# Performance work log

Measured on AMD Instinct MI355X. Metric: run time of the kernel, lower is better.

## Reference

```python
import jax, jax.numpy as jnp
import numpy as np

B, S, D, H, DH = 4, 2048, 512, 8, 64  # batch, seq, input_dim, heads, per-head output_dim


def setup_inputs() -> dict:
    key = jax.random.key(0)
    ks = jax.random.split(key, 10)
    scale = 0.02
    inp = {
        "x": jax.random.normal(ks[0], (B, S, D), dtype=jnp.float32),
        "biological_mask": jnp.ones((B, S), dtype=bool),
        "Wq": jax.random.normal(ks[1], (D, H * DH), dtype=jnp.float32) * scale,
        "bq": jnp.zeros((H * DH,), dtype=jnp.float32),
        "Wk": jax.random.normal(ks[2], (D, H * DH), dtype=jnp.float32) * scale,
        "bk": jnp.zeros((H * DH,), dtype=jnp.float32),
        "Wv": jax.random.normal(ks[3], (D, H * DH), dtype=jnp.float32) * scale,
        "bv": jnp.zeros((H * DH,), dtype=jnp.float32),
        "Wo": jax.random.normal(ks[4], (H * DH, DH), dtype=jnp.float32) * scale,
        "bo": jnp.zeros((DH,), dtype=jnp.float32),
        "prior_weight": jnp.full((1,), 0.1, dtype=jnp.float32),
    }
    return inp


def reference(x, biological_mask, Wq, bq, Wk, bk, Wv, bv, Wo, bo, prior_weight):
    b, s, _ = x.shape
    inv_sqrt_dh = jnp.float32(1.0 / np.sqrt(DH))
    # projections -> [B,H,S,DH]
    q = (x @ Wq + bq).reshape(b, s, H, DH).transpose(0, 2, 1, 3)
    k = (x @ Wk + bk).reshape(b, s, H, DH).transpose(0, 2, 1, 3)
    v = (x @ Wv + bv).reshape(b, s, H, DH).transpose(0, 2, 1, 3)
    # scores [B,H,S,S]
    scores = jnp.einsum("bhqd,bhkd->bhqk", q, k) * inv_sqrt_dh
    # biological prior: identity matrix, broadcast over batch and heads
    prior = jnp.eye(s, dtype=scores.dtype)[None, None, :, :]
    scores = scores + prior_weight[0] * prior
    attn = jax.nn.softmax(scores, axis=-1)  # dropout is identity in eval mode
    attended = jnp.einsum("bhqk,bhkd->bhqd", attn, v)
    attended = attended.transpose(0, 2, 1, 3).reshape(b, s, H * DH)
    return attended @ Wo + bo
```

## Files before the change

kernel.cpp:

```cpp
#include <hip/hip_runtime.h>
#include <hip/hip_bf16.h>

#define B_ 4
#define S_ 2048
#define D_ 512
#define H_ 8
#define DH_ 64
#define HD_ 512
#define M_ 8192
#define QKVN 1536
#define QKN 1024
#define LOG2E 1.4426950408889634f

typedef __attribute__((ext_vector_type(8))) short bf16x8;
typedef __attribute__((ext_vector_type(4))) float f32x4;
typedef unsigned short u16;

__device__ inline u16 f2bf(float f) {
    __hip_bfloat16 h = __float2bfloat16(f);
    return *reinterpret_cast<u16*>(&h);
}

__device__ inline void async_cp16(const void* g, void* l) {
    __builtin_amdgcn_global_load_lds(
        (const __attribute__((address_space(1))) unsigned int*)g,
        (__attribute__((address_space(3))) unsigned int*)l, 16, 0, 0);
}

__global__ __launch_bounds__(256) void prep_all(
    const float* __restrict__ x, const float* __restrict__ Wq,
    const float* __restrict__ Wk, const float* __restrict__ Wv,
    const float* __restrict__ Wo, u16* __restrict__ xb,
    u16* __restrict__ WqkvT, u16* __restrict__ WoT)
{
    const int z = blockIdx.z;
    const int tid = threadIdx.x;

    if (z == 4) {
        const int id = blockIdx.y * 64 + blockIdx.x;
#pragma unroll
        for (int it = 0; it < 4; ++it) {
            int i = it * 131072 + id * 256 + tid;
            float4 a = *reinterpret_cast<const float4*>(&x[(size_t)i * 8]);
            float4 b = *reinterpret_cast<const float4*>(&x[(size_t)i * 8 + 4]);
            bf16x8 o;
            o[0] = f2bf(a.x); o[1] = f2bf(a.y); o[2] = f2bf(a.z); o[3] = f2bf(a.w);
            o[4] = f2bf(b.x); o[5] = f2bf(b.y); o[6] = f2bf(b.z); o[7] = f2bf(b.w);
            *reinterpret_cast<bf16x8*>(&xb[(size_t)i * 8]) = o;
        }
        return;
    }

    const float* src; u16* dst; int R, C;
    if (z < 3) { if (blockIdx.x >= 8) return;
                 src = (z == 0) ? Wq : (z == 1) ? Wk : Wv;
                 dst = WqkvT + (size_t)z * 512 * 512; R = 512; C = 512; }
    else       { if (blockIdx.x) return; src = Wo; dst = WoT; R = 512; C = 64; }

    __shared__ u16 T[64][65];
    const int c0 = blockIdx.x * 64, r0 = blockIdx.y * 64;
#pragma unroll
    for (int i = 0; i < 4; ++i) {
        int idx = i * 256 + tid;
        int r = idx >> 4, q4 = (idx & 15) << 2;
        float4 vv = *reinterpret_cast<const float4*>(&src[(size_t)(r0 + r) * C + c0 + q4]);
        T[r][q4 + 0] = f2bf(vv.x); T[r][q4 + 1] = f2bf(vv.y);
        T[r][q4 + 2] = f2bf(vv.z); T[r][q4 + 3] = f2bf(vv.w);
    }
    __syncthreads();
#pragma unroll
    for (int i = 0; i < 2; ++i) {
        int idx = i * 256 + tid;
        int cc = idx >> 3, jj = idx & 7;
        bf16x8 o;
#pragma unroll
        for (int e = 0; e < 8; ++e) o[e] = (short)T[jj * 8 + e][cc];
        *reinterpret_cast<bf16x8*>(&dst[(size_t)(c0 + cc) * R + r0 + jj * 8]) = o;
    }
}

__global__ __launch_bounds__(256) void gemm_qkv(
    const u16* __restrict__ A, const u16* __restrict__ BT,
    const float* __restrict__ bq, const float* __restrict__ bk,
    const float* __restrict__ bv, u16* __restrict__ qk,
    u16* __restrict__ v3, float qscale)
{
    __shared__ __align__(16) u16 As[128 * 64];
    __shared__ __align__(16) u16 Bs[128 * 64];
    const int tid = threadIdx.x, lane = tid & 63, w = tid >> 6;
    const int l15 = lane & 15, l4 = lane >> 4;

    const int bidf = blockIdx.x;
    const int xcd = bidf & 7, pos = bidf >> 3;
    const int swz = xcd * 96 + pos;
    const int by = swz / 12, bx = swz - by * 12;
    const int tm = by * 128, tn = bx * 128;
    const int wm = (w >> 1) * 64, wn = (w & 1) * 64;

    f32x4 acc[4][4] = {};

    for (int k0 = 0; k0 < 512; k0 += 64) {
#pragma unroll
        for (int i = 0; i < 4; ++i) {
            int call = w * 4 + i;
            int c = call * 64 + lane;
            int r = c >> 3, j = c & 7;
            async_cp16(A + (size_t)(tm + r) * 512 + k0 + ((j ^ (r & 7)) << 3),
                       &As[call * 512]);
            async_cp16(BT + (size_t)(tn + r) * 512 + k0 + ((j ^ (r & 7)) << 3),
                       &Bs[call * 512]);
        }
        __syncthreads();
#pragma unroll
        for (int ks = 0; ks < 2; ++ks) {
            bf16x8 af[4], bf[4];
#pragma unroll
            for (int mf = 0; mf < 4; ++mf) {
                int r = wm + mf * 16 + l15;
                int j = ks * 4 + l4;
                af[mf] = *reinterpret_cast<const bf16x8*>(&As[(r * 8 + (j ^ (r & 7))) * 8]);
            }
#pragma unroll
            for (int nf = 0; nf < 4; ++nf) {
                int r = wn + nf * 16 + l15;
                int j = ks * 4 + l4;
                bf[nf] = *reinterpret_cast<const bf16x8*>(&Bs[(r * 8 + (j ^ (r & 7))) * 8]);
            }
#pragma unroll
            for (int mf = 0; mf < 4; ++mf)
#pragma unroll
                for (int nf = 0; nf < 4; ++nf)
                    acc[mf][nf] = __builtin_amdgcn_mfma_f32_16x16x32_bf16(
                        af[mf], bf[nf], acc[mf][nf], 0, 0, 0);
        }
        __syncthreads();
    }
#pragma unroll
    for (int nf = 0; nf < 4; ++nf) {
        const int col = tn + wn + nf * 16 + l15;
        if (col < QKN) {
            const float bias_v = (col < 512) ? bq[col] : bk[col - 512];
            const float scl = (col < 512) ? qscale : 1.0f;
#pragma unroll
            for (int mf = 0; mf < 4; ++mf)
#pragma unroll
                for (int r = 0; r < 4; ++r) {
                    int row = tm + wm + mf * 16 + l4 * 4 + r;
                    qk[(size_t)row * QKN + col] = f2bf((acc[mf][nf][r] + bias_v) * scl);
                }
        } else {
            const int dcol = col - QKN;
            const float bias_v = bv[dcol];
            const int hh = dcol >> 6, d64 = dcol & 63;
            const int n = d64 >> 4, dd = d64 & 15;
#pragma unroll
            for (int mf = 0; mf < 4; ++mf) {
                int row0 = tm + wm + mf * 16 + l4 * 4;
                int b = row0 >> 11, s = row0 & 2047;
                int t = s >> 6, s6 = s & 63;
                int ks = s6 >> 5, l4i = (s6 >> 3) & 3, kvi = s6 & 7;
                ushort4 pk;
                pk.x = f2bf(acc[mf][nf][0] + bias_v);
                pk.y = f2bf(acc[mf][nf][1] + bias_v);
                pk.z = f2bf(acc[mf][nf][2] + bias_v);
                pk.w = f2bf(acc[mf][nf][3] + bias_v);
                size_t idx = (((((size_t)(b * 8 + hh) * 32 + t) * 4 + n) * 2 + ks) * 4
                              + l4i) * 128 + dd * 8 + kvi;
                *reinterpret_cast<ushort4*>(&v3[idx]) = pk;
            }
        }
    }
}

__global__ __launch_bounds__(256, 4) void flash_mfma(
    const u16* __restrict__ qk, const u16* __restrict__ v3,
    const float* __restrict__ pw_ptr, u16* __restrict__ att)
{
    __shared__ __align__(16) u16 Kb[2][8192];

    const int tid = threadIdx.x, lane = tid & 63, w = tid >> 6;
    const int l15 = lane & 15, l4 = lane >> 4;
    const int bid = blockIdx.x;
    const int x = bid & 7, g = bid >> 3;
    const int bh = x * 4 + (g >> 5), qt = g & 31;
    const int h = bh & 7, b = bh >> 3;
    const float pwl = pw_ptr[0] * LOG2E;

    const u16* qbase = qk + (size_t)b * S_ * QKN + h * 64;
    const u16* kbase = qbase + 512;
    const u16* vbase = v3 + (size_t)bh * 32 * 4 * 2 * 512 + l4 * 128 + l15 * 8;

    const int qrow0 = qt * 64 + w * 16;
    bf16x8 qb[2];
#pragma unroll
    for (int ks2 = 0; ks2 < 2; ++ks2)
        qb[ks2] = *reinterpret_cast<const bf16x8*>(
            &qbase[(size_t)(qrow0 + l15) * QKN + ks2 * 32 + l4 * 8]);

    const bf16x8 ones = {(short)0x3F80, (short)0x3F80, (short)0x3F80, (short)0x3F80,
                         (short)0x3F80, (short)0x3F80, (short)0x3F80, (short)0x3F80};

    f32x4 accv[4] = {};
    f32x4 accl = {};

#define STAGE2(buf, jj) do {                                                       \
    _Pragma("unroll")                                                              \
    for (int i_ = 0; i_ < 4; ++i_) {                                               \
        int call_ = w * 4 + i_;                                                    \
        int c_ = call_ * 64 + lane;                                                \
        int rho_ = c_ >> 3, j_ = c_ & 7;                                           \
        int r6_ = rho_ & 63;                                                       \
        int pi_ = (rho_ & 64) | (r6_ & 32) | ((r6_ & 12) << 1)                     \
                | ((r6_ & 16) >> 2) | (r6_ & 3);                                   \
        async_cp16(kbase + (size_t)((jj) + pi_) * QKN + ((j_ ^ (r6_ & 7)) << 3),   \
                   &Kb[buf][call_ * 512]);                                         \
    } } while (0)

    STAGE2(0, 0);
    __syncthreads();
    int cur = 0;

    for (int t = 0; t < 16; ++t) {
        if (t < 15) STAGE2(cur ^ 1, (t + 1) << 7);

#pragma unroll
        for (int half = 0; half < 2; ++half) {
            const int t2 = t * 2 + half;
            const int j0h = t2 << 6;
            const u16* vt = vbase + (size_t)t2 * 4096;
            const u16* kb = &Kb[cur][half * 4096];

            bf16x8 vb01[2][2];
#pragma unroll
            for (int n = 0; n < 2; ++n)
#pragma unroll
                for (int ks = 0; ks < 2; ++ks)
                    vb01[n][ks] = *reinterpret_cast<const bf16x8*>(
                        vt + (n * 2 + ks) * 512);

            f32x4 s[4] = {};
            __builtin_amdgcn_s_setprio(1);
#pragma unroll
            for (int c = 0; c < 4; ++c)
#pragma unroll
                for (int ks2 = 0; ks2 < 2; ++ks2) {
                    const int rr = c * 16 + l15;
                    const int sl = ks2 * 4 + l4;
                    bf16x8 ka = *reinterpret_cast<const bf16x8*>(
                        &kb[(rr * 8 + (sl ^ (rr & 7))) * 8]);
                    s[c] = __builtin_amdgcn_mfma_f32_16x16x32_bf16(ka, qb[ks2], s[c], 0, 0, 0);
                }
            __builtin_amdgcn_s_setprio(0);

            bf16x8 vb23[2][2];
#pragma unroll
            for (int n = 0; n < 2; ++n)
#pragma unroll
                for (int ks = 0; ks < 2; ++ks)
                    vb23[n][ks] = *reinterpret_cast<const bf16x8*>(
                        vt + ((n + 2) * 2 + ks) * 512);

            if (t2 == qt) {
#pragma unroll
                for (int c = 0; c < 4; ++c)
#pragma unroll
                    for (int r = 0; r < 4; ++r) {
                        int kv = (c >> 1) * 32 + l4 * 8 + (c & 1) * 4 + r;
                        if (j0h + kv == qrow0 + l15) s[c][r] += pwl;
                    }
            }

            bf16x8 pa[2];
#pragma unroll
            for (int ks = 0; ks < 2; ++ks)
#pragma unroll
                for (int d2 = 0; d2 < 2; ++d2)
#pragma unroll
                    for (int r = 0; r < 4; ++r)
                        pa[ks][d2 * 4 + r] = (short)f2bf(exp2f(s[ks * 2 + d2][r]));

            __builtin_amdgcn_s_setprio(1);
            accl = __builtin_amdgcn_mfma_f32_16x16x32_bf16(pa[0], ones, accl, 0, 0, 0);
            accl = __builtin_amdgcn_mfma_f32_16x16x32_bf16(pa[1], ones, accl, 0, 0, 0);
#pragma unroll
            for (int n = 0; n < 2; ++n)
#pragma unroll
                for (int ks = 0; ks < 2; ++ks)
                    accv[n] = __builtin_amdgcn_mfma_f32_16x16x32_bf16(
                        pa[ks], vb01[n][ks], accv[n], 0, 0, 0);
#pragma unroll
            for (int n = 0; n < 2; ++n)
#pragma unroll
                for (int ks = 0; ks < 2; ++ks)
                    accv[n + 2] = __builtin_amdgcn_mfma_f32_16x16x32_bf16(
                        pa[ks], vb23[n][ks], accv[n + 2], 0, 0, 0);
            __builtin_amdgcn_s_setprio(0);
        }

        __syncthreads();
        cur ^= 1;
    }
#undef STAGE2

#pragma unroll
    for (int r = 0; r < 4; ++r) {
        float inv = 1.0f / accl[r];
        int row = qrow0 + l4 * 4 + r;
#pragma unroll
        for (int nf = 0; nf < 4; ++nf)
            att[(size_t)(b * S_ + row) * HD_ + h * 64 + nf * 16 + l15] =
                f2bf(accv[nf][r] * inv);
    }
}

__global__ __launch_bounds__(256) void out_proj(
    const u16* __restrict__ att, const u16* __restrict__ WoT,
    const float* __restrict__ bo, float* __restrict__ out)
{
    __shared__ float red[32][65];
    const int tid = threadIdx.x, lane = tid & 63, w = tid >> 6;
    const int l15 = lane & 15, l4 = lane >> 4;
    const int row0 = blockIdx.x * 32;
    const int rsub = (w & 1) * 16, kh = w >> 1;

    f32x4 acc[4] = {};
#pragma unroll
    for (int ks = 0; ks < 8; ++ks) {
        bf16x8 a = *reinterpret_cast<const bf16x8*>(
            &att[(size_t)(row0 + rsub + l15) * 512 + (kh * 8 + ks) * 32 + l4 * 8]);
#pragma unroll
        for (int nf = 0; nf < 4; ++nf) {
            bf16x8 bb = *reinterpret_cast<const bf16x8*>(
                &WoT[(size_t)(nf * 16 + l15) * 512 + (kh * 8 + ks) * 32 + l4 * 8]);
            acc[nf] = __builtin_amdgcn_mfma_f32_16x16x32_bf16(a, bb, acc[nf], 0, 0, 0);
        }
    }
    if (kh == 1) {
#pragma unroll
        for (int nf = 0; nf < 4; ++nf)
#pragma unroll
            for (int r = 0; r < 4; ++r)
                red[rsub + l4 * 4 + r][nf * 16 + l15] = acc[nf][r];
    }
    __syncthreads();
    if (kh == 0) {
#pragma unroll
        for (int nf = 0; nf < 4; ++nf) {
            int n = nf * 16 + l15;
            float bias_v = bo[n];
#pragma unroll
            for (int r = 0; r < 4; ++r)
                out[(size_t)(row0 + rsub + l4 * 4 + r) * 64 + n] =
                    acc[nf][r] + red[rsub + l4 * 4 + r][n] + bias_v;
        }
    }
}

extern "C" void kernel_launch(void* const* d_in, const int* in_sizes, int n_in,
                              void* d_out, int out_size, void* d_ws, size_t ws_size,
                              hipStream_t stream)
{
    const float* x  = (const float*)d_in[0];
    const float* Wq = (const float*)d_in[2];
    const float* bq = (const float*)d_in[3];
    const float* Wk = (const float*)d_in[4];
    const float* bk = (const float*)d_in[5];
    const float* Wv = (const float*)d_in[6];
    const float* bv = (const float*)d_in[7];
    const float* Wo = (const float*)d_in[8];
    const float* bo = (const float*)d_in[9];
    const float* pw = (const float*)d_in[10];

    u16* ws = (u16*)d_ws;
    size_t o = 0;
    u16* xb    = ws + o; o += (size_t)M_ * D_;
    u16* WqkvT = ws + o; o += (size_t)QKVN * D_;
    u16* WoT   = ws + o; o += (size_t)DH_ * HD_;
    u16* qkb   = ws + o; o += (size_t)M_ * QKN;
    u16* v3b   = ws + o; o += (size_t)M_ * HD_;
    u16* att   = ws + o; o += (size_t)M_ * HD_;

    dim3 blk(256);
    prep_all<<<dim3(64, 8, 5), blk, 0, stream>>>(x, Wq, Wk, Wv, Wo, xb, WqkvT, WoT);

    gemm_qkv<<<dim3(768), blk, 0, stream>>>(
        xb, WqkvT, bq, bk, bv, qkb, v3b, 0.125f * LOG2E);

    flash_mfma<<<dim3(1024), blk, 0, stream>>>(qkb, v3b, pw, att);

    out_proj<<<dim3(256), blk, 0, stream>>>(att, WoT, bo, (float*)d_out);
}
```

Before: 98.87 us.

## Split attention KV range into two halves with separate combine kernel

Each query tile's KV loop is split across two blocks (split-K / flash-decoding style), doubling the grid to 2048 blocks with half the LDS per block and a higher occupancy hint. Each block writes an unnormalized bf16 partial output plus row sums, and a new combine kernel adds the two partials and normalizes. Because the softmax uses no running max (the scores are small), partials can simply be added. The aim is more parallelism and occupancy, at the cost of an extra launch, extra global traffic for the partials, and an extra bf16 rounding step.

```diff
diff --git a/kernel.cpp b/kernel.cpp
--- a/kernel.cpp
+++ b/kernel.cpp
@@ -15,10 +15,14 @@
 typedef __attribute__((ext_vector_type(8))) short bf16x8;
 typedef __attribute__((ext_vector_type(4))) float f32x4;
 typedef unsigned short u16;
+typedef unsigned int u32;
 
 __device__ inline u16 f2bf(float f) {
     __hip_bfloat16 h = __float2bfloat16(f);
     return *reinterpret_cast<u16*>(&h);
+}
+__device__ inline float bf2f(u16 u) {
+    union { u32 i; float f; } v; v.i = (u32)u << 16; return v.f;
 }
 
 __device__ inline void async_cp16(const void* g, void* l) {
@@ -172,17 +176,19 @@
     }
 }
 
-__global__ __launch_bounds__(256, 4) void flash_mfma(
+__global__ __launch_bounds__(256, 8) void flash_mfma(
     const u16* __restrict__ qk, const u16* __restrict__ v3,
-    const float* __restrict__ pw_ptr, u16* __restrict__ att)
-{
-    __shared__ __align__(16) u16 Kb[2][8192];
+    const float* __restrict__ pw_ptr, u16* __restrict__ opart,
+    float* __restrict__ lpart)
+{
+    __shared__ __align__(16) u16 Kb[2][4096];
 
     const int tid = threadIdx.x, lane = tid & 63, w = tid >> 6;
     const int l15 = lane & 15, l4 = lane >> 4;
     const int bid = blockIdx.x;
     const int x = bid & 7, g = bid >> 3;
-    const int bh = x * 4 + (g >> 5), qt = g & 31;
+    const int bh = x * 4 + (g >> 6);
+    const int rem = g & 63, qt = rem >> 1, half = rem & 1;
     const int h = bh & 7, b = bh >> 3;
     const float pwl = pw_ptr[0] * LOG2E;
 
@@ -202,114 +208,139 @@
 
     f32x4 accv[4] = {};
     f32x4 accl = {};
-
-#define STAGE2(buf, jj) do {                                                       \
+    const int t0 = half * 16;
+
+#define STAGE(buf, jj) do {                                                        \
     _Pragma("unroll")                                                              \
-    for (int i_ = 0; i_ < 4; ++i_) {                                               \
-        int call_ = w * 4 + i_;                                                    \
+    for (int i_ = 0; i_ < 2; ++i_) {                                               \
+        int call_ = w * 2 + i_;                                                    \
         int c_ = call_ * 64 + lane;                                                \
         int rho_ = c_ >> 3, j_ = c_ & 7;                                           \
-        int r6_ = rho_ & 63;                                                       \
-        int pi_ = (rho_ & 64) | (r6_ & 32) | ((r6_ & 12) << 1)                     \
-                | ((r6_ & 16) >> 2) | (r6_ & 3);                                   \
-        async_cp16(kbase + (size_t)((jj) + pi_) * QKN + ((j_ ^ (r6_ & 7)) << 3),   \
+        int pi_ = (rho_ & 32) | ((rho_ & 12) << 1) | ((rho_ & 16) >> 2)            \
+                | (rho_ & 3);                                                      \
+        async_cp16(kbase + (size_t)((jj) + pi_) * QKN + ((j_ ^ (rho_ & 7)) << 3),  \
                    &Kb[buf][call_ * 512]);                                         \
     } } while (0)
 
-    STAGE2(0, 0);
+    STAGE(0, t0 << 6);
     __syncthreads();
     int cur = 0;
 
-    for (int t = 0; t < 16; ++t) {
-        if (t < 15) STAGE2(cur ^ 1, (t + 1) << 7);
-
-#pragma unroll
-        for (int half = 0; half < 2; ++half) {
-            const int t2 = t * 2 + half;
-            const int j0h = t2 << 6;
-            const u16* vt = vbase + (size_t)t2 * 4096;
-            const u16* kb = &Kb[cur][half * 4096];
-
-            bf16x8 vb01[2][2];
-#pragma unroll
-            for (int n = 0; n < 2; ++n)
-#pragma unroll
-                for (int ks = 0; ks < 2; ++ks)
-                    vb01[n][ks] = *reinterpret_cast<const bf16x8*>(
-                        vt + (n * 2 + ks) * 512);
-
-            f32x4 s[4] = {};
-            __builtin_amdgcn_s_setprio(1);
+    for (int ti = 0; ti < 16; ++ti) {
+        const int t = t0 + ti;
+        const int j0 = t << 6;
+        const u16* vt = vbase + (size_t)t * 4096;
+
+        bf16x8 vb01[2][2];
+#pragma unroll
+        for (int n = 0; n < 2; ++n)
+#pragma unroll
+            for (int ks = 0; ks < 2; ++ks)
+                vb01[n][ks] = *reinterpret_cast<const bf16x8*>(
+                    vt + (n * 2 + ks) * 512);
+
+        if (ti < 15) STAGE(cur ^ 1, (t + 1) << 6);
+
+        f32x4 s[4] = {};
+        __builtin_amdgcn_s_setprio(1);
+#pragma unroll
+        for (int c = 0; c < 4; ++c)
+#pragma unroll
+            for (int ks2 = 0; ks2 < 2; ++ks2) {
+                const int rr = c * 16 + l15;
+                const int sl = ks2 * 4 + l4;
+                bf16x8 ka = *reinterpret_cast<const bf16x8*>(
+                    &Kb[cur][(rr * 8 + (sl ^ (rr & 7))) * 8]);
+                s[c] = __builtin_amdgcn_mfma_f32_16x16x32_bf16(ka, qb[ks2], s[c], 0, 0, 0);
+            }
+        __builtin_amdgcn_s_setprio(0);
+
+        bf16x8 vb23[2][2];
+#pragma unroll
+        for (int n = 0; n < 2; ++n)
+#pragma unroll
+            for (int ks = 0; ks < 2; ++ks)
+                vb23[n][ks] = *reinterpret_cast<const bf16x8*>(
+                    vt + ((n + 2) * 2 + ks) * 512);
+
+        if (t == qt) {
 #pragma unroll
             for (int c = 0; c < 4; ++c)
 #pragma unroll
-                for (int ks2 = 0; ks2 < 2; ++ks2) {
-                    const int rr = c * 16 + l15;
-                    const int sl = ks2 * 4 + l4;
-                    bf16x8 ka = *reinterpret_cast<const bf16x8*>(
-                        &kb[(rr * 8 + (sl ^ (rr & 7))) * 8]);
-                    s[c] = __builtin_amdgcn_mfma_f32_16x16x32_bf16(ka, qb[ks2], s[c], 0, 0, 0);
+                for (int r = 0; r < 4; ++r) {
+                    int kv = (c >> 1) * 32 + l4 * 8 + (c & 1) * 4 + r;
+                    if (j0 + kv == qrow0 + l15) s[c][r] += pwl;
                 }
-            __builtin_amdgcn_s_setprio(0);
-
-            bf16x8 vb23[2][2];
-#pragma unroll
-            for (int n = 0; n < 2; ++n)
-#pragma unroll
-                for (int ks = 0; ks < 2; ++ks)
-                    vb23[n][ks] = *reinterpret_cast<const bf16x8*>(
-                        vt + ((n + 2) * 2 + ks) * 512);
-
-            if (t2 == qt) {
-#pragma unroll
-                for (int c = 0; c < 4; ++c)
-#pragma unroll
-                    for (int r = 0; r < 4; ++r) {
-                        int kv = (c >> 1) * 32 + l4 * 8 + (c & 1) * 4 + r;
-                        if (j0h + kv == qrow0 + l15) s[c][r] += pwl;
-                    }
-            }
-
-            bf16x8 pa[2];
+        }
+
+        bf16x8 pa[2];
+#pragma unroll
+        for (int ks = 0; ks < 2; ++ks)
+#pragma unroll
+            for (int d2 = 0; d2 < 2; ++d2)
+#pragma unroll
+                for (int r = 0; r < 4; ++r)
+                    pa[ks][d2 * 4 + r] = (short)f2bf(exp2f(s[ks * 2 + d2][r]));
+
+        __builtin_amdgcn_s_setprio(1);
+        accl = __builtin_amdgcn_mfma_f32_16x16x32_bf16(pa[0], ones, accl, 0, 0, 0);
+        accl = __builtin_amdgcn_mfma_f32_16x16x32_bf16(pa[1], ones, accl, 0, 0, 0);
+#pragma unroll
+        for (int n = 0; n < 2; ++n)
 #pragma unroll
             for (int ks = 0; ks < 2; ++ks)
-#pragma unroll
-                for (int d2 = 0; d2 < 2; ++d2)
-#pragma unroll
-                    for (int r = 0; r < 4; ++r)
-                        pa[ks][d2 * 4 + r] = (short)f2bf(exp2f(s[ks * 2 + d2][r]));
-
-            __builtin_amdgcn_s_setprio(1);
-            accl = __builtin_amdgcn_mfma_f32_16x16x32_bf16(pa[0], ones, accl, 0, 0, 0);
-            accl = __builtin_amdgcn_mfma_f32_16x16x32_bf16(pa[1], ones, accl, 0, 0, 0);
-#pragma unroll
-            for (int n = 0; n < 2; ++n)
-#pragma unroll
-                for (int ks = 0; ks < 2; ++ks)
-                    accv[n] = __builtin_amdgcn_mfma_f32_16x16x32_bf16(
-                        pa[ks], vb01[n][ks], accv[n], 0, 0, 0);
-#pragma unroll
-            for (int n = 0; n < 2; ++n)
-#pragma unroll
-                for (int ks = 0; ks < 2; ++ks)
-                    accv[n + 2] = __builtin_amdgcn_mfma_f32_16x16x32_bf16(
-                        pa[ks], vb23[n][ks], accv[n + 2], 0, 0, 0);
-            __builtin_amdgcn_s_setprio(0);
-        }
+                accv[n] = __builtin_amdgcn_mfma_f32_16x16x32_bf16(
+                    pa[ks], vb01[n][ks], accv[n], 0, 0, 0);
+#pragma unroll
+        for (int n = 0; n < 2; ++n)
+#pragma unroll
+            for (int ks = 0; ks < 2; ++ks)
+                accv[n + 2] = __builtin_amdgcn_mfma_f32_16x16x32_bf16(
+                    pa[ks], vb23[n][ks], accv[n + 2], 0, 0, 0);
+        __builtin_amdgcn_s_setprio(0);
 
         __syncthreads();
         cur ^= 1;
     }
-#undef STAGE2
-
+#undef STAGE
+
+    const size_t cell = (size_t)(bh * 32 + qt) * 2 + half;
 #pragma unroll
     for (int r = 0; r < 4; ++r) {
-        float inv = 1.0f / accl[r];
-        int row = qrow0 + l4 * 4 + r;
+        const int row6 = w * 16 + l4 * 4 + r;
 #pragma unroll
         for (int nf = 0; nf < 4; ++nf)
-            att[(size_t)(b * S_ + row) * HD_ + h * 64 + nf * 16 + l15] =
-                f2bf(accv[nf][r] * inv);
+            opart[cell * 4096 + (size_t)row6 * 64 + nf * 16 + l15] =
+                f2bf(accv[nf][r]);
+        if (l15 == 0) lpart[cell * 64 + row6] = accl[r];
+    }
+}
+
+__global__ __launch_bounds__(256) void combine(
+    const u16* __restrict__ opart, const float* __restrict__ lpart,
+    u16* __restrict__ att)
+{
+    const int cp = blockIdx.x;
+    const int bh = cp >> 5, qt = cp & 31;
+    const int h = bh & 7, b = bh >> 3;
+    const int tid = threadIdx.x;
+    const int row = tid >> 2, cg = tid & 3;
+
+    const float inv = 1.0f / (lpart[(size_t)cp * 128 + row] +
+                              lpart[(size_t)cp * 128 + 64 + row]);
+    const u16* p0 = opart + (size_t)cp * 8192 + (size_t)row * 64 + cg * 16;
+    const u16* p1 = p0 + 4096;
+
+    u16* dst = att + ((size_t)(b * S_ + qt * 64 + row)) * HD_ + h * 64 + cg * 16;
+#pragma unroll
+    for (int hchunk = 0; hchunk < 2; ++hchunk) {
+        bf16x8 a = *reinterpret_cast<const bf16x8*>(p0 + hchunk * 8);
+        bf16x8 c = *reinterpret_cast<const bf16x8*>(p1 + hchunk * 8);
+        bf16x8 o;
+#pragma unroll
+        for (int e = 0; e < 8; ++e)
+            o[e] = (short)f2bf((bf2f((u16)a[e]) + bf2f((u16)c[e])) * inv);
+        *reinterpret_cast<bf16x8*>(dst + hchunk * 8) = o;
     }
 }
 
@@ -379,6 +410,8 @@
     u16* qkb   = ws + o; o += (size_t)M_ * QKN;
     u16* v3b   = ws + o; o += (size_t)M_ * HD_;
     u16* att   = ws + o; o += (size_t)M_ * HD_;
+    u16* opart = ws + o; o += (size_t)2048 * 4096;
+    float* lprt = (float*)(ws + o); o += (size_t)2048 * 64 * 2;
 
     dim3 blk(256);
     prep_all<<<dim3(64, 8, 5), blk, 0, stream>>>(x, Wq, Wk, Wv, Wo, xb, WqkvT, WoT);
@@ -386,7 +419,9 @@
     gemm_qkv<<<dim3(768), blk, 0, stream>>>(
         xb, WqkvT, bq, bk, bv, qkb, v3b, 0.125f * LOG2E);
 
-    flash_mfma<<<dim3(1024), blk, 0, stream>>>(qkb, v3b, pw, att);
+    flash_mfma<<<dim3(2048), blk, 0, stream>>>(qkb, v3b, pw, opart, lprt);
+
+    combine<<<dim3(1024), blk, 0, stream>>>(opart, lprt, att);
 
     out_proj<<<dim3(256), blk, 0, stream>>>(att, WoT, bo, (float*)d_out);
 }
```

Result: slower. 366.4 us (+270.6%).
